# Kernel tuning notes

Hardware: AMD Instinct MI355X
Metric: run time of the kernel (lower is better)

## Reference

```python
import jax, jax.numpy as jnp
import numpy as np

B, N, DIM = 4, 2048, 64  # batch, seq_len (== gate out dim), model dim (== dim_head)
H, DH = 8, 64            # heads, dim_head


def setup_inputs() -> dict:
    key = jax.random.key(0)
    ks = jax.random.split(key, 12)
    inner = H * DH
    inp = {
        'q': jax.random.normal(ks[0], (B, N, DIM), jnp.float32),
        'k': jax.random.normal(ks[1], (B, N, DIM), jnp.float32),
        'v': jax.random.normal(ks[2], (B, N, DIM), jnp.float32),
        'Wq': jax.random.normal(ks[3], (inner, DIM), jnp.float32) * 0.05,
        'Wk': jax.random.normal(ks[4], (inner, DIM), jnp.float32) * 0.05,
        'Wv': jax.random.normal(ks[5], (inner, DIM), jnp.float32) * 0.05,
        'Wo': jax.random.normal(ks[6], (DIM, inner), jnp.float32) * 0.05,
        'bo': jax.random.normal(ks[7], (DIM,), jnp.float32) * 0.05,
        'Wg': jax.random.normal(ks[8], (N, DIM), jnp.float32) * 0.05,
        's_local': jnp.float32(1.0),
        's_long': jnp.float32(1.0),
        # recurrent compressive-memory state; positive to avoid 0/0 of zero-init buffers
        'mem': jax.random.uniform(ks[9], (H, DH, DH), jnp.float32) + 0.5,
        'mem_norm': jax.random.uniform(ks[10], (H, N, 1), jnp.float32) + 0.5,
    }
    return inp


def _heads(x, W):
    # x: (B,N,DIM) @ W.T (DIM, H*DH) -> (B,H,N,DH)
    y = x @ W.T
    return y.reshape(x.shape[0], x.shape[1], H, DH).transpose(0, 2, 1, 3)


def reference(q, k, v, Wq, Wk, Wv, Wo, bo, Wg, s_local, s_long, mem, mem_norm):
    scale = DH ** -0.5
    qh, kh, vh = _heads(q, Wq), _heads(k, Wk), _heads(v, Wv)  # (B,H,N,DH)

    # local softmax attention, down-gated by (1 - sigmoid(local scalar))
    sim = jnp.einsum('bhnd,bhmd->bhnm', qh, kh) * scale
    local_attn = jax.nn.softmax(sim, axis=-1) * (1.0 - jax.nn.sigmoid(s_local))

    # query compressive memory: elu(q) @ M / (elu(q) * norm)
    eq = jax.nn.elu(qh)
    mem_q = jnp.einsum('bhnd,hde->bhne', eq, mem) / (eq * mem_norm[None])  # (B,H,N,DH)
    gated = jax.nn.sigmoid(s_long) * jnp.einsum('bhnd,md->bhnm', mem_q, Wg)  # (B,H,N,N)

    attn = local_attn + gated
    out = jnp.einsum('bhnm,bhmd->bhnd', attn, vh)
    out = out.transpose(0, 2, 1, 3).reshape(q.shape[0], q.shape[1], H * DH)
    out = out @ Wo.T + bo  # (B,N,DIM)

    # memory update (state side effect in the original forward)
    ek = jax.nn.elu(kh)
    v_term = vh - jnp.einsum('bhnd,hde->bhne', ek, mem) / (ek * mem_norm[None])
    new_mem = mem[None] + jnp.einsum('bhnd,bhne->bhde', ek, v_term)  # (B,H,DH,DH)
    new_norm = ek.sum(-1)  # (B,H,N)
    return out, new_mem, new_norm
```

## Files before the change

### kernel.cpp

```cpp
#include <hip/hip_runtime.h>
#include <math.h>


#define B_   4
#define N_   2048
#define H_   8
#define BH_  32
#define KP   72
#define KPV  68
#define SCLK 0.18033688f

typedef __bf16 bf16x8 __attribute__((ext_vector_type(8)));
typedef __bf16 bf16x4 __attribute__((ext_vector_type(4)));
typedef short  s16x4  __attribute__((ext_vector_type(4)));
typedef float  f32x4  __attribute__((ext_vector_type(4)));

__device__ __forceinline__ float eluf(float x) {
    return x > 0.0f ? x : expm1f(x);
}

__device__ __forceinline__ float fexp2(float x) {
    return __builtin_amdgcn_exp2f(x);
}

__device__ __forceinline__ f32x4 mfma16(bf16x4 a, bf16x4 b, f32x4 c) {
#if __has_builtin(__builtin_amdgcn_mfma_f32_16x16x16_bf16)
    return __builtin_amdgcn_mfma_f32_16x16x16_bf16(a, b, c, 0, 0, 0);
#else
    s16x4 ai, bi;
    __builtin_memcpy(&ai, &a, 8);
    __builtin_memcpy(&bi, &b, 8);
    return __builtin_amdgcn_mfma_f32_16x16x16bf16_1k(ai, bi, c, 0, 0, 0);
#endif
}

__global__ __launch_bounds__(256) void k_proj(
    const float* __restrict__ q, const float* __restrict__ k, const float* __restrict__ v,
    const float* __restrict__ Wq, const float* __restrict__ Wk, const float* __restrict__ Wv,
    __bf16* __restrict__ qb, float* __restrict__ kh, __bf16* __restrict__ kb,
    __bf16* __restrict__ vb, __bf16* __restrict__ vbT)
{
    const int which = blockIdx.z;
    const int h    = blockIdx.y;
    const int row0 = blockIdx.x * 64;
    const int tid  = threadIdx.x;
    const int b = row0 >> 11, nb = row0 & 2047;

    __shared__ __align__(16) float  AsT[64][68];
    __shared__ __align__(16) float  WsT[64][68];
    __shared__ __align__(16) __bf16 Cs[64 * 72];

    if (which == 2) {
        const int w = tid >> 6, lane = tid & 63;
        const int quad = lane >> 4, m = lane & 15;
        const float* ar = v + (size_t)(row0 + w * 16 + m) * 64;
        bf16x8 a0, a1;
        #pragma unroll
        for (int j = 0; j < 8; ++j) {
            a0[j] = (__bf16)ar[quad * 8 + j];
            a1[j] = (__bf16)ar[32 + quad * 8 + j];
        }
        f32x4 acc[4];
        #pragma unroll
        for (int t = 0; t < 4; ++t) {
            const float* wr = Wv + (size_t)(h * 64 + t * 16 + m) * 64;
            bf16x8 b0, b1;
            #pragma unroll
            for (int j = 0; j < 8; ++j) {
                b0[j] = (__bf16)wr[quad * 8 + j];
                b1[j] = (__bf16)wr[32 + quad * 8 + j];
            }
            f32x4 z = {0.f, 0.f, 0.f, 0.f};
            z = __builtin_amdgcn_mfma_f32_16x16x32_bf16(a0, b0, z, 0, 0, 0);
            acc[t] = __builtin_amdgcn_mfma_f32_16x16x32_bf16(a1, b1, z, 0, 0, 0);
        }
        #pragma unroll
        for (int t = 0; t < 4; ++t)
            #pragma unroll
            for (int r = 0; r < 4; ++r)
                Cs[(w * 16 + quad * 4 + r) * 72 + t * 16 + m] = (__bf16)acc[t][r];
        __syncthreads();
        const int rr = tid >> 2, csg = (tid & 3) * 16;
        bf16x8 r0 = *(const bf16x8*)&Cs[rr * 72 + csg];
        bf16x8 r1 = *(const bf16x8*)&Cs[rr * 72 + csg + 8];
        size_t gb = ((((size_t)b * H_ + h) * N_ + nb + rr) << 6) + csg;
        *(bf16x8*)&vb[gb]     = r0;
        *(bf16x8*)&vb[gb + 8] = r1;
        const int e = tid >> 2, ns = (tid & 3) * 16;
        bf16x8 t0, t1;
        #pragma unroll
        for (int j = 0; j < 8; ++j) {
            t0[j] = Cs[(ns + j) * 72 + e];
            t1[j] = Cs[(ns + 8 + j) * 72 + e];
        }
        size_t base = (((size_t)b * H_ + h) * 64 + e) * (size_t)N_ + nb + ns;
        *(bf16x8*)&vbT[base]     = t0;
        *(bf16x8*)&vbT[base + 8] = t1;
        return;
    }

    const float* __restrict__ src = (which == 0) ? q : k;
    const float* __restrict__ W   = (which == 0) ? Wq : Wk;
    for (int s = 0; s < 16; ++s) {
        int flat = s * 256 + tid;
        int r = flat >> 6, d = flat & 63;
        AsT[d][r] = src[(size_t)(row0 + r) * 64 + d];
        WsT[d][r] = W[(size_t)(h * 64 + r) * 64 + d];
    }
    __syncthreads();

    const int ty = tid >> 4, tx = tid & 15;
    float acc[4][4];
    #pragma unroll
    for (int i = 0; i < 4; ++i)
        #pragma unroll
        for (int j = 0; j < 4; ++j) acc[i][j] = 0.0f;
    for (int kd = 0; kd < 64; ++kd) {
        float4 a4 = *(const float4*)&AsT[kd][ty * 4];
        float4 w4 = *(const float4*)&WsT[kd][tx * 4];
        float a[4] = {a4.x, a4.y, a4.z, a4.w};
        float w[4] = {w4.x, w4.y, w4.z, w4.w};
        #pragma unroll
        for (int i = 0; i < 4; ++i)
            #pragma unroll
            for (int j = 0; j < 4; ++j) acc[i][j] = fmaf(a[i], w[j], acc[i][j]);
    }

    if (which == 0) {
        #pragma unroll
        for (int i = 0; i < 4; ++i) {
            size_t idx = ((((size_t)b * H_ + h) * N_ + nb + ty * 4 + i) << 6) + tx * 4;
            bf16x4 o4 = {(__bf16)acc[i][0], (__bf16)acc[i][1],
                         (__bf16)acc[i][2], (__bf16)acc[i][3]};
            *(bf16x4*)&qb[idx] = o4;
        }
    } else {
        #pragma unroll
        for (int i = 0; i < 4; ++i) {
            size_t idx = ((((size_t)b * H_ + h) * N_ + nb + ty * 4 + i) << 6) + tx * 4;
            *(float4*)&kh[idx] = make_float4(acc[i][0], acc[i][1], acc[i][2], acc[i][3]);
            bf16x4 o4 = {(__bf16)(acc[i][0] * SCLK), (__bf16)(acc[i][1] * SCLK),
                         (__bf16)(acc[i][2] * SCLK), (__bf16)(acc[i][3] * SCLK)};
            *(bf16x4*)&kb[idx] = o4;
        }
    }
}

__global__ __launch_bounds__(256) void k_memacc(
    const float* __restrict__ kh, const __bf16* __restrict__ vb,
    const float* __restrict__ mem, const float* __restrict__ mem_norm,
    float* __restrict__ pmem, float* __restrict__ out_norm)
{
    const int chunk = blockIdx.x;
    const int bh    = blockIdx.y;
    const int h     = bh & 7;
    const int n0    = chunk * 128;

    __shared__ __align__(16) __bf16 memT_hi[64 * KP], memT_lo[64 * KP];
    __shared__ __align__(16) __bf16 ekn_hi[64 * KP],  ekn_lo[64 * KP];
    __shared__ __align__(16) __bf16 ekT_hi[64 * KP],  ekT_lo[64 * KP];
    __shared__ __align__(16) __bf16 vtT_hi[64 * KP],  vtT_lo[64 * KP];

    const int tid  = threadIdx.x;
    const int w    = tid >> 6, lane = tid & 63;
    const int quad = lane >> 4, m = lane & 15;

    for (int s = 0; s < 16; ++s) {
        int flat = s * 256 + tid;
        int d = flat >> 6, e = flat & 63;
        float mv = mem[(size_t)h * 4096 + flat];
        __bf16 hi = (__bf16)mv;
        memT_hi[e * KP + d] = hi;
        memT_lo[e * KP + d] = (__bf16)(mv - (float)hi);
    }

    bf16x8 onesv;
    #pragma unroll
    for (int j = 0; j < 8; ++j) onesv[j] = (m == 0) ? (__bf16)1.0f : (__bf16)0.0f;

    f32x4 accM[4];
    #pragma unroll
    for (int t = 0; t < 4; ++t) { f32x4 z = {0.f, 0.f, 0.f, 0.f}; accM[t] = z; }
    __syncthreads();

    for (int sub = 0; sub < 2; ++sub) {
        const int nb = n0 + sub * 64;
        for (int rr = w; rr < 64; rr += 4) {
            const int n = nb + rr;
            float ekv = eluf(kh[((size_t)bh * N_ + n) * 64 + lane]);
            __bf16 hi = (__bf16)ekv;
            __bf16 lo = (__bf16)(ekv - (float)hi);
            ekn_hi[rr * KP + lane] = hi;
            ekn_lo[rr * KP + lane] = lo;
            ekT_hi[lane * KP + rr] = hi;
            ekT_lo[lane * KP + rr] = lo;
        }
        __syncthreads();

        f32x4 km[4];
        #pragma unroll
        for (int t = 0; t < 4; ++t) { f32x4 z = {0.f, 0.f, 0.f, 0.f}; km[t] = z; }
        f32x4 nsum = {0.f, 0.f, 0.f, 0.f};
        #pragma unroll
        for (int c2 = 0; c2 < 2; ++c2) {
            bf16x8 Ah = *(const bf16x8*)&ekn_hi[(w * 16 + m) * KP + c2 * 32 + quad * 8];
            bf16x8 Al = *(const bf16x8*)&ekn_lo[(w * 16 + m) * KP + c2 * 32 + quad * 8];
            nsum = __builtin_amdgcn_mfma_f32_16x16x32_bf16(Ah, onesv, nsum, 0, 0, 0);
            nsum = __builtin_amdgcn_mfma_f32_16x16x32_bf16(Al, onesv, nsum, 0, 0, 0);
            #pragma unroll
            for (int et = 0; et < 4; ++et) {
                bf16x8 Bh = *(const bf16x8*)&memT_hi[(et * 16 + m) * KP + c2 * 32 + quad * 8];
                bf16x8 Bl = *(const bf16x8*)&memT_lo[(et * 16 + m) * KP + c2 * 32 + quad * 8];
                km[et] = __builtin_amdgcn_mfma_f32_16x16x32_bf16(Al, Bh, km[et], 0, 0, 0);
                km[et] = __builtin_amdgcn_mfma_f32_16x16x32_bf16(Ah, Bl, km[et], 0, 0, 0);
                km[et] = __builtin_amdgcn_mfma_f32_16x16x32_bf16(Ah, Bh, km[et], 0, 0, 0);
            }
        }
        if (m == 0) {
            #pragma unroll
            for (int r = 0; r < 4; ++r)
                out_norm[(size_t)bh * N_ + nb + w * 16 + quad * 4 + r] = nsum[r];
        }
        float nrmv[4];
        #pragma unroll
        for (int r = 0; r < 4; ++r)
            nrmv[r] = mem_norm[(size_t)h * N_ + nb + w * 16 + quad * 4 + r];
        #pragma unroll
        for (int et = 0; et < 4; ++et) {
            #pragma unroll
            for (int r = 0; r < 4; ++r) {
                const int nl = w * 16 + quad * 4 + r;
                const int e  = et * 16 + m;
                float vh  = (float)vb[((size_t)bh * N_ + nb + nl) * 64 + e];
                float ekv = (float)ekn_hi[nl * KP + e] + (float)ekn_lo[nl * KP + e];
                float vt  = vh - km[et][r] * __builtin_amdgcn_rcpf(ekv * nrmv[r]);
                __bf16 hi = (__bf16)vt;
                vtT_hi[e * KP + nl] = hi;
                vtT_lo[e * KP + nl] = (__bf16)(vt - (float)hi);
            }
        }
        __syncthreads();

        #pragma unroll
        for (int c2 = 0; c2 < 2; ++c2) {
            bf16x8 Ah = *(const bf16x8*)&ekT_hi[(w * 16 + m) * KP + c2 * 32 + quad * 8];
            bf16x8 Al = *(const bf16x8*)&ekT_lo[(w * 16 + m) * KP + c2 * 32 + quad * 8];
            #pragma unroll
            for (int et = 0; et < 4; ++et) {
                bf16x8 Bh = *(const bf16x8*)&vtT_hi[(et * 16 + m) * KP + c2 * 32 + quad * 8];
                bf16x8 Bl = *(const bf16x8*)&vtT_lo[(et * 16 + m) * KP + c2 * 32 + quad * 8];
                accM[et] = __builtin_amdgcn_mfma_f32_16x16x32_bf16(Al, Bh, accM[et], 0, 0, 0);
                accM[et] = __builtin_amdgcn_mfma_f32_16x16x32_bf16(Ah, Bl, accM[et], 0, 0, 0);
                accM[et] = __builtin_amdgcn_mfma_f32_16x16x32_bf16(Ah, Bh, accM[et], 0, 0, 0);
            }
        }
        __syncthreads();
    }

    const size_t base = ((size_t)chunk * BH_ + bh) * 4096;
    #pragma unroll
    for (int et = 0; et < 4; ++et)
        #pragma unroll
        for (int r = 0; r < 4; ++r)
            pmem[base + (size_t)(w * 16 + quad * 4 + r) * 64 + et * 16 + m] =
                accM[et][r];
}

__global__ __launch_bounds__(256) void k_gv(
    const float* __restrict__ Wg, const __bf16* __restrict__ vbT,
    float* __restrict__ pGv)
{
    const int chunk = blockIdx.x;
    const int bh    = blockIdx.y;
    const int n0    = chunk * 128;
    __shared__ __align__(16) __bf16 WgT[64 * 136];
    const int tid  = threadIdx.x;
    const int w    = tid >> 6, lane = tid & 63;
    const int quad = lane >> 4, m = tid & 15;

    for (int s = 0; s < 8; ++s) {
        int f4 = s * 256 + tid;
        int n = f4 >> 4, dg = (f4 & 15) * 4;
        float4 wv = *(const float4*)&Wg[(size_t)(n0 + n) * 64 + dg];
        WgT[(dg + 0) * 136 + n] = (__bf16)wv.x;
        WgT[(dg + 1) * 136 + n] = (__bf16)wv.y;
        WgT[(dg + 2) * 136 + n] = (__bf16)wv.z;
        WgT[(dg + 3) * 136 + n] = (__bf16)wv.w;
    }
    __syncthreads();

    f32x4 acc[4];
    #pragma unroll
    for (int t = 0; t < 4; ++t) { f32x4 z = {0.f, 0.f, 0.f, 0.f}; acc[t] = z; }
    #pragma unroll
    for (int c = 0; c < 4; ++c) {
        bf16x8 Af = *(const bf16x8*)&WgT[(w * 16 + m) * 136 + c * 32 + quad * 8];
        #pragma unroll
        for (int et = 0; et < 4; ++et) {
            bf16x8 Bf = *(const bf16x8*)&vbT[((size_t)bh * 64 + et * 16 + m) * N_ +
                                             n0 + c * 32 + quad * 8];
            acc[et] = __builtin_amdgcn_mfma_f32_16x16x32_bf16(Af, Bf, acc[et], 0, 0, 0);
        }
    }
    const size_t base = ((size_t)chunk * BH_ + bh) * 4096;
    #pragma unroll
    for (int et = 0; et < 4; ++et)
        #pragma unroll
        for (int r = 0; r < 4; ++r)
            pGv[base + (size_t)(w * 16 + quad * 4 + r) * 64 + et * 16 + m] =
                acc[et][r];
}

__global__ __launch_bounds__(256) void k_reduce(
    const float* __restrict__ mem, const float* __restrict__ pmem,
    const float* __restrict__ pGv, float* __restrict__ out_mem, float* __restrict__ Gv)
{
    const int idx = blockIdx.x * 256 + threadIdx.x;
    const int bh = idx >> 12, h = bh & 7, de = idx & 4095;
    float sm = mem[(size_t)h * 4096 + de];
    float sg = 0.0f;
    #pragma unroll
    for (int c = 0; c < 16; ++c) {
        sm += pmem[(size_t)c * 131072 + idx];
        sg += pGv[(size_t)c * 131072 + idx];
    }
    out_mem[idx] = sm;
    Gv[idx] = sg;
}

__global__ __launch_bounds__(512, 2) void k_flash(
    const __bf16* __restrict__ qb, const __bf16* __restrict__ kb,
    const __bf16* __restrict__ vbT, const float* __restrict__ mem,
    const float* __restrict__ mem_norm, const float* __restrict__ Gv,
    const float* __restrict__ s_local_p, const float* __restrict__ s_long_p,
    __bf16* __restrict__ o)
{
    const int n0 = blockIdx.x * 256;
    const int bh = blockIdx.y;
    const int h  = bh & 7;
    const __bf16* __restrict__ kbp = kb  + (size_t)bh * N_ * 64;
    const __bf16* __restrict__ vtp = vbT + (size_t)bh * 64 * N_;

    __shared__ __align__(16) char smem[56832];
    __bf16* const KbA = (__bf16*)(smem);
    __bf16* const KbB = (__bf16*)(smem + 9216);
    __bf16* const VTA = (__bf16*)(smem + 18432);
    __bf16* const VTB = (__bf16*)(smem + 27136);
    __bf16* const MT  = (__bf16*)(smem);
    __bf16* const GT  = (__bf16*)(smem + 9216);
    __bf16* const Pw  = (__bf16*)(smem + 17920);
    float*  const lsl   = (float*)(smem + 54784);
    float*  const nrm_l = (float*)(smem + 55808);

    const int tid  = threadIdx.x;
    const int w    = tid >> 6, lane = tid & 63;
    const int quad = lane >> 4, m = lane & 15;
    const float gl   = 1.0f - 1.0f / (1.0f + __expf(-s_local_p[0]));
    const float sigg = 1.0f / (1.0f + __expf(-s_long_p[0]));

    if (tid < 256) nrm_l[tid] = mem_norm[(size_t)h * N_ + n0 + tid];

    const size_t q0 = ((size_t)bh * N_ + n0 + w * 32 + m) * 64;
    const size_t q1 = q0 + 16 * 64;
    bf16x8 qa00 = *(const bf16x8*)&qb[q0 + quad * 8];
    bf16x8 qa01 = *(const bf16x8*)&qb[q0 + 32 + quad * 8];
    bf16x8 qa10 = *(const bf16x8*)&qb[q1 + quad * 8];
    bf16x8 qa11 = *(const bf16x8*)&qb[q1 + 32 + quad * 8];

    f32x4 O0[4], O1[4];
    #pragma unroll
    for (int t = 0; t < 4; ++t) {
        f32x4 z = {0.f, 0.f, 0.f, 0.f};
        O0[t] = z; O1[t] = z;
    }
    float lsum0 = 0.f, lsum1 = 0.f;
    const int pr0 = w * 32, pr1 = w * 32 + 16;

    const int srow = tid >> 3, scg = (tid & 7) * 8;
    bf16x8 pk0 = *(const bf16x8*)&kbp[(size_t)srow * 64 + scg];
    bf16x8 pv0 = *(const bf16x8*)&vtp[(size_t)srow * N_ + scg];
    *(bf16x8*)&KbA[srow * KP + scg]  = pk0;
    *(bf16x8*)&VTA[srow * KPV + scg] = pv0;
    {
        const size_t kn = (size_t)(64 + srow) * 64 + scg;
        const size_t vn = (size_t)srow * N_ + 64 + scg;
        pk0 = *(const bf16x8*)&kbp[kn];
        pv0 = *(const bf16x8*)&vtp[vn];
    }

    for (int c = 0; c < 32; ++c) {
        __syncthreads();
        if (c + 1 < 32) {
            __bf16* Kn = (c & 1) ? KbA : KbB;
            __bf16* Vn = (c & 1) ? VTA : VTB;
            *(bf16x8*)&Kn[srow * KP + scg]  = pk0;
            *(bf16x8*)&Vn[srow * KPV + scg] = pv0;
        }
        if (c + 2 < 32) {
            const size_t kn = (size_t)((c + 2) * 64 + srow) * 64 + scg;
            const size_t vn = (size_t)srow * N_ + (c + 2) * 64 + scg;
            pk0 = *(const bf16x8*)&kbp[kn];
            pv0 = *(const bf16x8*)&vtp[vn];
        }
        const __bf16* Kc = (c & 1) ? KbB : KbA;
        const __bf16* Vc = (c & 1) ? VTB : VTA;

        f32x4 s0[4], s1[4];
        #pragma unroll
        for (int t = 0; t < 4; ++t) {
            bf16x8 ka0 = *(const bf16x8*)&Kc[(t * 16 + m) * KP + quad * 8];
            bf16x8 ka1 = *(const bf16x8*)&Kc[(t * 16 + m) * KP + 32 + quad * 8];
            f32x4 z = {0.f, 0.f, 0.f, 0.f};
            z = __builtin_amdgcn_mfma_f32_16x16x32_bf16(ka0, qa00, z, 0, 0, 0);
            s0[t] = __builtin_amdgcn_mfma_f32_16x16x32_bf16(ka1, qa01, z, 0, 0, 0);
            f32x4 z2 = {0.f, 0.f, 0.f, 0.f};
            z2 = __builtin_amdgcn_mfma_f32_16x16x32_bf16(ka0, qa10, z2, 0, 0, 0);
            s1[t] = __builtin_amdgcn_mfma_f32_16x16x32_bf16(ka1, qa11, z2, 0, 0, 0);
        }

        bf16x4 pa0[4], pa1[4];
        #pragma unroll
        for (int t = 0; t < 4; ++t) {
            float p0 = fexp2(s0[t][0]), p1 = fexp2(s0[t][1]);
            float p2 = fexp2(s0[t][2]), p3 = fexp2(s0[t][3]);
            lsum0 += p0 + p1 + p2 + p3;
            bf16x4 pk = {(__bf16)p0, (__bf16)p1, (__bf16)p2, (__bf16)p3};
            pa0[t] = pk;
            float r0 = fexp2(s1[t][0]), r1 = fexp2(s1[t][1]);
            float r2 = fexp2(s1[t][2]), r3 = fexp2(s1[t][3]);
            lsum1 += r0 + r1 + r2 + r3;
            bf16x4 rk = {(__bf16)r0, (__bf16)r1, (__bf16)r2, (__bf16)r3};
            pa1[t] = rk;
        }

        #pragma unroll
        for (int t = 0; t < 4; ++t) {
            #pragma unroll
            for (int et = 0; et < 4; ++et) {
                bf16x4 vb4 = *(const bf16x4*)&Vc[(et * 16 + m) * KPV + t * 16 + quad * 4];
                O0[et] = mfma16(pa0[t], vb4, O0[et]);
                O1[et] = mfma16(pa1[t], vb4, O1[et]);
            }
        }
    }

    lsum0 += __shfl_xor(lsum0, 16, 64); lsum0 += __shfl_xor(lsum0, 32, 64);
    lsum1 += __shfl_xor(lsum1, 16, 64); lsum1 += __shfl_xor(lsum1, 32, 64);
    if (lane < 16) { lsl[pr0 + lane] = lsum0; lsl[pr1 + lane] = lsum1; }

    __syncthreads();
    {
        const float* mp = mem + (size_t)h * 4096;
        const float* gp = Gv + (size_t)bh * 4096;
        #pragma unroll
        for (int s2 = 0; s2 < 2; ++s2) {
            int idx = s2 * 512 + tid;
            int e = idx & 63, d4 = (idx >> 6) << 2;
            bf16x4 mv, gv;
            #pragma unroll
            for (int j = 0; j < 4; ++j) {
                mv[j] = (__bf16)mp[(size_t)(d4 + j) * 64 + e];
                gv[j] = (__bf16)gp[(size_t)(d4 + j) * 64 + e];
            }
            *(bf16x4*)&MT[e * KP + d4] = mv;
            *(bf16x4*)&GT[e * KPV + d4] = gv;
        }
    }
    __syncthreads();

    __bf16* op = o + ((size_t)bh * N_ + n0) * 64;
    #pragma unroll
    for (int s = 0; s < 2; ++s) {
        const int prs = w * 32 + s * 16;
        bf16x8 ea0, ea1;
        #pragma unroll
        for (int j = 0; j < 8; ++j) {
            ea0[j] = (__bf16)eluf((float)(s == 0 ? qa00[j] : qa10[j]));
            ea1[j] = (__bf16)eluf((float)(s == 0 ? qa01[j] : qa11[j]));
        }
        f32x4 num[4];
        #pragma unroll
        for (int t = 0; t < 4; ++t) {
            bf16x8 b0 = *(const bf16x8*)&MT[(t * 16 + m) * KP + quad * 8];
            bf16x8 b1 = *(const bf16x8*)&MT[(t * 16 + m) * KP + 32 + quad * 8];
            f32x4 z = {0.f, 0.f, 0.f, 0.f};
            z = __builtin_amdgcn_mfma_f32_16x16x32_bf16(ea0, b0, z, 0, 0, 0);
            num[t] = __builtin_amdgcn_mfma_f32_16x16x32_bf16(ea1, b1, z, 0, 0, 0);
        }
        *(bf16x8*)&Pw[(prs + m) * KP + quad * 8]      = ea0;
        *(bf16x8*)&Pw[(prs + m) * KP + 32 + quad * 8] = ea1;
        asm volatile("s_waitcnt lgkmcnt(0)" ::: "memory");
        float mq[4][4];
        #pragma unroll
        for (int t = 0; t < 4; ++t)
            #pragma unroll
            for (int r = 0; r < 4; ++r) {
                float eqv = (float)Pw[(prs + quad * 4 + r) * KP + t * 16 + m];
                mq[t][r] = num[t][r] / (eqv * nrm_l[prs + quad * 4 + r]);
            }
        #pragma unroll
        for (int t = 0; t < 4; ++t)
            #pragma unroll
            for (int r = 0; r < 4; ++r)
                Pw[(prs + quad * 4 + r) * KP + t * 16 + m] = (__bf16)mq[t][r];
        asm volatile("s_waitcnt lgkmcnt(0)" ::: "memory");
        bf16x8 ma0 = *(const bf16x8*)&Pw[(prs + m) * KP + quad * 8];
        bf16x8 ma1 = *(const bf16x8*)&Pw[(prs + m) * KP + 32 + quad * 8];

        #pragma unroll
        for (int t = 0; t < 4; ++t) {
            bf16x8 g0 = *(const bf16x8*)&GT[(t * 16 + m) * KPV + quad * 8];
            bf16x8 g1 = *(const bf16x8*)&GT[(t * 16 + m) * KPV + 32 + quad * 8];
            f32x4 z = {0.f, 0.f, 0.f, 0.f};
            z = __builtin_amdgcn_mfma_f32_16x16x32_bf16(ma0, g0, z, 0, 0, 0);
            f32x4 o2 = __builtin_amdgcn_mfma_f32_16x16x32_bf16(ma1, g1, z, 0, 0, 0);
            #pragma unroll
            for (int r = 0; r < 4; ++r) {
                const int qr = prs + quad * 4 + r;
                float val = ((s == 0) ? O0[t][r] : O1[t][r]) * (gl / lsl[qr])
                            + sigg * o2[r];
                op[(size_t)qr * 64 + t * 16 + m] = (__bf16)val;
            }
        }
    }
}

__global__ __launch_bounds__(256) void k_outproj(
    const __bf16* __restrict__ o, const float* __restrict__ Wo,
    const float* __restrict__ bo, float* __restrict__ out)
{
    const int row0 = blockIdx.x * 64;
    const int b = row0 >> 11, nb = row0 & 2047;
    __shared__ __align__(16) __bf16 WoS[64 * 40];
    const int tid  = threadIdx.x;
    const int w    = tid >> 6, lane = tid & 63;
    const int quad = lane >> 4, m = lane & 15;

    f32x4 acc[4];
    #pragma unroll
    for (int t = 0; t < 4; ++t) { f32x4 z = {0.f, 0.f, 0.f, 0.f}; acc[t] = z; }

    for (int kbk = 0; kbk < 16; ++kbk) {
        for (int s2 = 0; s2 < 8; ++s2) {
            int flat = s2 * 256 + tid;
            int n = flat >> 5, kk = flat & 31;
            WoS[n * 40 + kk] = (__bf16)Wo[(size_t)n * 512 + kbk * 32 + kk];
        }
        __syncthreads();
        const int hc = kbk >> 1;
        size_t arow = (((size_t)b * H_ + hc) * N_ + nb + w * 16 + m);
        bf16x8 af = *(const bf16x8*)&o[arow * 64 + (kbk & 1) * 32 + quad * 8];
        #pragma unroll
        for (int t = 0; t < 4; ++t) {
            bf16x8 bf_ = *(const bf16x8*)&WoS[(t * 16 + m) * 40 + quad * 8];
            acc[t] = __builtin_amdgcn_mfma_f32_16x16x32_bf16(af, bf_, acc[t], 0, 0, 0);
        }
        __syncthreads();
    }
    #pragma unroll
    for (int t = 0; t < 4; ++t) {
        float bias = bo[t * 16 + m];
        #pragma unroll
        for (int r = 0; r < 4; ++r)
            out[(size_t)(row0 + w * 16 + quad * 4 + r) * 64 + t * 16 + m] =
                acc[t][r] + bias;
    }
}

extern "C" void kernel_launch(void* const* d_in, const int* in_sizes, int n_in,
                              void* d_out, int out_size, void* d_ws, size_t ws_size,
                              hipStream_t stream)
{
    const float* q        = (const float*)d_in[0];
    const float* k        = (const float*)d_in[1];
    const float* v        = (const float*)d_in[2];
    const float* Wq       = (const float*)d_in[3];
    const float* Wk       = (const float*)d_in[4];
    const float* Wv       = (const float*)d_in[5];
    const float* Wo       = (const float*)d_in[6];
    const float* bo       = (const float*)d_in[7];
    const float* Wg       = (const float*)d_in[8];
    const float* s_local  = (const float*)d_in[9];
    const float* s_long   = (const float*)d_in[10];
    const float* mem      = (const float*)d_in[11];
    const float* mem_norm = (const float*)d_in[12];

    float* ws = (float*)d_ws;
    float*  kh  = ws;
    __bf16* qb  = (__bf16*)(ws + 4194304);
    __bf16* kb  = (__bf16*)(ws + 6291456);
    __bf16* vb  = (__bf16*)(ws + 8388608);
    __bf16* vbT = (__bf16*)(ws + 10485760);
    float*  Gv  = ws + 12582912;
    float*  pm  = ws + 12713984;
    float*  pg  = ws + 14811136;
    __bf16* o   = (__bf16*)(ws + 12713984);

    float* out      = (float*)d_out;
    float* out_mem  = out + 524288;
    float* out_norm = out + 655360;

    k_proj   <<<dim3(128, 8, 3), 256, 0, stream>>>(q, k, v, Wq, Wk, Wv,
                                                   qb, kh, kb, vb, vbT);
    k_memacc <<<dim3(16, 32),    256, 0, stream>>>(kh, vb, mem, mem_norm,
                                                   pm, out_norm);
    k_gv     <<<dim3(16, 32),    256, 0, stream>>>(Wg, vbT, pg);
    k_reduce <<<dim3(512),       256, 0, stream>>>(mem, pm, pg, out_mem, Gv);
    k_flash  <<<dim3(8, 32),     512, 0, stream>>>(qb, kb, vbT, mem, mem_norm, Gv,
                                                   s_local, s_long, o);
    k_outproj<<<dim3(128),       256, 0, stream>>>(o, Wo, bo, out);
}
```

Baseline: 198.8 us.

## Compute softmax row sums via MFMA, set wave priorities, restage Wo in halves

In the attention loop the per-lane exp sums and the final shuffle reduction are replaced by an extra MFMA against a ones vector, so the row sums come out of the matrix unit directly. The loop barrier becomes an explicit lgkmcnt wait plus s_barrier, and s_setprio raises wave priority around the MFMA sections. The output projection now loads Wo as float4 in two 256-wide halves instead of sixteen scalar-loaded 32-wide slices, which cuts barriers and global loads at the cost of more shared memory. The row sums now add up bf16-rounded probabilities rather than fp32 values, which slightly changes numerics.

```diff
diff --git a/kernel.cpp b/kernel.cpp
--- a/kernel.cpp
+++ b/kernel.cpp
@@ -373,7 +373,10 @@
         f32x4 z = {0.f, 0.f, 0.f, 0.f};
         O0[t] = z; O1[t] = z;
     }
-    float lsum0 = 0.f, lsum1 = 0.f;
+    f32x4 nacc0 = {0.f, 0.f, 0.f, 0.f}, nacc1 = {0.f, 0.f, 0.f, 0.f};
+    bf16x4 ones4;
+    #pragma unroll
+    for (int j = 0; j < 4; ++j) ones4[j] = (m == 0) ? (__bf16)1.0f : (__bf16)0.0f;
     const int pr0 = w * 32, pr1 = w * 32 + 16;
 
     const int srow = tid >> 3, scg = (tid & 7) * 8;
@@ -389,7 +392,8 @@
     }
 
     for (int c = 0; c < 32; ++c) {
-        __syncthreads();
+        asm volatile("s_waitcnt lgkmcnt(0)" ::: "memory");
+        __builtin_amdgcn_s_barrier();
         if (c + 1 < 32) {
             __bf16* Kn = (c & 1) ? KbA : KbB;
             __bf16* Vn = (c & 1) ? VTA : VTB;
@@ -406,6 +410,7 @@
         const __bf16* Vc = (c & 1) ? VTB : VTA;
 
         f32x4 s0[4], s1[4];
+        __builtin_amdgcn_s_setprio(1);
         #pragma unroll
         for (int t = 0; t < 4; ++t) {
             bf16x8 ka0 = *(const bf16x8*)&Kc[(t * 16 + m) * KP + quad * 8];
@@ -417,24 +422,26 @@
             z2 = __builtin_amdgcn_mfma_f32_16x16x32_bf16(ka0, qa10, z2, 0, 0, 0);
             s1[t] = __builtin_amdgcn_mfma_f32_16x16x32_bf16(ka1, qa11, z2, 0, 0, 0);
         }
+        __builtin_amdgcn_s_setprio(0);
 
         bf16x4 pa0[4], pa1[4];
         #pragma unroll
         for (int t = 0; t < 4; ++t) {
             float p0 = fexp2(s0[t][0]), p1 = fexp2(s0[t][1]);
             float p2 = fexp2(s0[t][2]), p3 = fexp2(s0[t][3]);
-            lsum0 += p0 + p1 + p2 + p3;
             bf16x4 pk = {(__bf16)p0, (__bf16)p1, (__bf16)p2, (__bf16)p3};
             pa0[t] = pk;
             float r0 = fexp2(s1[t][0]), r1 = fexp2(s1[t][1]);
             float r2 = fexp2(s1[t][2]), r3 = fexp2(s1[t][3]);
-            lsum1 += r0 + r1 + r2 + r3;
             bf16x4 rk = {(__bf16)r0, (__bf16)r1, (__bf16)r2, (__bf16)r3};
             pa1[t] = rk;
         }
 
+        __builtin_amdgcn_s_setprio(1);
         #pragma unroll
         for (int t = 0; t < 4; ++t) {
+            nacc0 = mfma16(pa0[t], ones4, nacc0);
+            nacc1 = mfma16(pa1[t], ones4, nacc1);
             #pragma unroll
             for (int et = 0; et < 4; ++et) {
                 bf16x4 vb4 = *(const bf16x4*)&Vc[(et * 16 + m) * KPV + t * 16 + quad * 4];
@@ -442,11 +449,16 @@
                 O1[et] = mfma16(pa1[t], vb4, O1[et]);
             }
         }
-    }
-
-    lsum0 += __shfl_xor(lsum0, 16, 64); lsum0 += __shfl_xor(lsum0, 32, 64);
-    lsum1 += __shfl_xor(lsum1, 16, 64); lsum1 += __shfl_xor(lsum1, 32, 64);
-    if (lane < 16) { lsl[pr0 + lane] = lsum0; lsl[pr1 + lane] = lsum1; }
+        __builtin_amdgcn_s_setprio(0);
+    }
+
+    if (m == 0) {
+        #pragma unroll
+        for (int r = 0; r < 4; ++r) {
+            lsl[pr0 + quad * 4 + r] = nacc0[r];
+            lsl[pr1 + quad * 4 + r] = nacc1[r];
+        }
+    }
 
     __syncthreads();
     {
@@ -531,7 +543,7 @@
 {
     const int row0 = blockIdx.x * 64;
     const int b = row0 >> 11, nb = row0 & 2047;
-    __shared__ __align__(16) __bf16 WoS[64 * 40];
+    __shared__ __align__(16) __bf16 WoS[64 * 296];
     const int tid  = threadIdx.x;
     const int w    = tid >> 6, lane = tid & 63;
     const int quad = lane >> 4, m = lane & 15;
@@ -540,20 +552,25 @@
     #pragma unroll
     for (int t = 0; t < 4; ++t) { f32x4 z = {0.f, 0.f, 0.f, 0.f}; acc[t] = z; }
 
-    for (int kbk = 0; kbk < 16; ++kbk) {
-        for (int s2 = 0; s2 < 8; ++s2) {
-            int flat = s2 * 256 + tid;
-            int n = flat >> 5, kk = flat & 31;
-            WoS[n * 40 + kk] = (__bf16)Wo[(size_t)n * 512 + kbk * 32 + kk];
+    for (int half = 0; half < 2; ++half) {
+        for (int s2 = 0; s2 < 16; ++s2) {
+            int f4 = s2 * 256 + tid;
+            int n = f4 >> 6, k4 = (f4 & 63) * 4;
+            float4 wv = *(const float4*)&Wo[(size_t)n * 512 + half * 256 + k4];
+            bf16x4 o4 = {(__bf16)wv.x, (__bf16)wv.y, (__bf16)wv.z, (__bf16)wv.w};
+            *(bf16x4*)&WoS[n * 296 + k4] = o4;
         }
         __syncthreads();
-        const int hc = kbk >> 1;
-        size_t arow = (((size_t)b * H_ + hc) * N_ + nb + w * 16 + m);
-        bf16x8 af = *(const bf16x8*)&o[arow * 64 + (kbk & 1) * 32 + quad * 8];
-        #pragma unroll
-        for (int t = 0; t < 4; ++t) {
-            bf16x8 bf_ = *(const bf16x8*)&WoS[(t * 16 + m) * 40 + quad * 8];
-            acc[t] = __builtin_amdgcn_mfma_f32_16x16x32_bf16(af, bf_, acc[t], 0, 0, 0);
+        for (int kbk = 0; kbk < 8; ++kbk) {
+            const int kbk2 = half * 8 + kbk;
+            const int hc = kbk2 >> 1;
+            size_t arow = (((size_t)b * H_ + hc) * N_ + nb + w * 16 + m);
+            bf16x8 af = *(const bf16x8*)&o[arow * 64 + (kbk2 & 1) * 32 + quad * 8];
+            #pragma unroll
+            for (int t = 0; t < 4; ++t) {
+                bf16x8 bf_ = *(const bf16x8*)&WoS[(t * 16 + m) * 296 + kbk * 32 + quad * 8];
+                acc[t] = __builtin_amdgcn_mfma_f32_16x16x32_bf16(af, bf_, acc[t], 0, 0, 0);
+            }
         }
         __syncthreads();
     }
```

New measurement: 202.6 us. No clear change (+1.9%).
